# Kernel tuning notes

Measured on AMD Instinct MI355X. Metric: run time of the kernel, lower is better.

Reference implementation:

```python
import jax, jax.numpy as jnp
import numpy as np

N, NC, G, C = 80000, 8000, 16, 5
E, ES = 160000, 80000
NUM_OPS, OP_E, OP_F, CFG_F, H = 120, 32, 140, 18, 32
ALPHA = 0.2  # tf.nn.leaky_relu default slope

seg = jax.ops.segment_sum

def lrelu(x):
    return jnp.where(x >= 0, x, ALPHA * x)

def l2norm(x):
    s = jnp.sum(x * x, axis=-1, keepdims=True)
    return x * jax.lax.rsqrt(jnp.maximum(s, 1e-12))

def setup_inputs():
    k = jax.random.split(jax.random.key(0), 20)
    p = lambda i, shp, s=0.1: jax.random.normal(k[i], shp, jnp.float32) * s
    d_in = CFG_F + OP_F + OP_E  # 190: concat(config, op feats, op embed)
    d_gc = CFG_F + H            # 50: concat(config, hidden)
    return {
        'op_feats': jax.random.normal(k[0], (N, OP_F), jnp.float32),
        'config_feats': jax.random.normal(k[1], (NC, C, CFG_F), jnp.float32),
        'op_ids': jax.random.randint(k[2], (N,), 0, NUM_OPS),
        'selected': jax.random.randint(k[3], (N,), 0, 2) == 1,
        'feed_src': jax.random.randint(k[4], (E,), 0, N),
        'feed_dst': jax.random.randint(k[5], (E,), 0, N),
        'sfeed_src': jax.random.randint(k[6], (ES,), 0, N),
        'sfeed_dst': jax.random.randint(k[7], (ES,), 0, N),
        'config_src': jnp.arange(NC),
        'config_dst': jax.random.randint(k[8], (NC,), 0, N),
        'sconfig_src': jnp.arange(NC),
        'sconfig_dst': jax.random.randint(k[9], (NC,), 0, N),
        'op_gid': (jnp.arange(N) * G) // N,
        'cfg_gid': (jnp.arange(NC) * G) // NC,
        'emb': p(10, (NUM_OPS, OP_E), 1.0),
        'pre_w1': p(11, (d_in, H)), 'pre_b1': jnp.zeros((H,), jnp.float32),
        'pre_w2': p(12, (H, H)), 'pre_b2': jnp.zeros((H,), jnp.float32),
        'gc1_w1': p(13, (d_gc, H)), 'gc1_b1': jnp.zeros((H,), jnp.float32),
        'gc1_w2': p(14, (H, H)), 'gc1_b2': jnp.zeros((H,), jnp.float32),
        'gc2_w1': p(15, (d_gc, H)), 'gc2_b1': jnp.zeros((H,), jnp.float32),
        'gc2_w2': p(16, (H, H)), 'gc2_b2': jnp.zeros((H,), jnp.float32),
        'post_w1': p(17, (3 * H, H)),
        'post_w2': p(18, (H, 1)),
    }

def _mlp(x, w1, b1, w2, b2):
    return lrelu(x @ w1 + b1) @ w2 + b2

def _node_forward(nf, cf, src, dst, csrc, cdst, pre, gcs):
    # AdjacencyMultiplier('config') @ config_feats : scatter nconfig feats to ops
    cfg = 100.0 * seg(cf[csrc], cdst, num_segments=N)            # [N, C, 18]
    x = jnp.broadcast_to(nf[:, None, :], (N, C, nf.shape[-1]))   # stack over configs
    x = lrelu(_mlp(jnp.concatenate([cfg, x], -1), *pre))         # prenet + leaky_relu
    # A_hat = A + A^T + I with symmetric normalization D^-1/2 A_hat D^-1/2
    loop = jnp.arange(N)
    src_all = jnp.concatenate([src, dst, loop])
    dst_all = jnp.concatenate([dst, src, loop])
    inv = jax.lax.rsqrt(seg(jnp.ones(src_all.shape, nf.dtype), dst_all, num_segments=N))
    inv = inv[:, None, None]
    for gp in gcs:
        y = jnp.concatenate([cfg, x], -1) * inv
        y = seg(y[src_all], dst_all, num_segments=N) * inv       # A_hat_norm @ y
        x = x + lrelu(_mlp(y, *gp))                              # residual
    return x

def _forward(op_feats, config_feats, emb, pre, gc1, gc2, post_w1, post_w2,
             op_ids, selected, feed, sfeed, cfg_e, scfg_e, op_gid, cfg_gid):
    nf = jnp.concatenate([op_feats, emb[op_ids]], -1)            # [N, 172]
    x_full = _node_forward(jax.lax.stop_gradient(nf), jax.lax.stop_gradient(config_feats),
                           feed[0], feed[1], cfg_e[0], cfg_e[1], pre, (gc1, gc2))
    x_bp = _node_forward(nf, config_feats, sfeed[0], sfeed[1],
                         scfg_e[0], scfg_e[1], pre, (gc1, gc2))
    x = jnp.where(selected[:, None, None], x_bp, x_full)         # [N, C, H]
    cfg_nodes = seg(x[cfg_e[1]], cfg_e[0], num_segments=NC)      # adj_config^T @ x
    op_sum = seg(x, op_gid, num_segments=G)                      # [G, C, H]
    cnt = seg(jnp.ones((N,), x.dtype), op_gid, num_segments=G)
    op_mean = op_sum / cnt[:, None, None]
    cfg_sum = seg(cfg_nodes, cfg_gid, num_segments=G)
    feats = jnp.concatenate([op_mean, l2norm(op_sum), l2norm(cfg_sum)], -1)  # [G, C, 3H]
    return (lrelu(feats @ post_w1) @ post_w2)[..., 0]            # [G, C]

def reference(op_feats, config_feats, op_ids, selected, feed_src, feed_dst,
              sfeed_src, sfeed_dst, config_src, config_dst, sconfig_src, sconfig_dst,
              op_gid, cfg_gid, emb, pre_w1, pre_b1, pre_w2, pre_b2,
              gc1_w1, gc1_b1, gc1_w2, gc1_b2, gc2_w1, gc2_b1, gc2_w2, gc2_b2,
              post_w1, post_w2):
    return _forward(op_feats, config_feats, emb,
                    (pre_w1, pre_b1, pre_w2, pre_b2),
                    (gc1_w1, gc1_b1, gc1_w2, gc1_b2),
                    (gc2_w1, gc2_b1, gc2_w2, gc2_b2),
                    post_w1, post_w2,
                    op_ids, selected, (feed_src, feed_dst), (sfeed_src, sfeed_dst),
                    (config_src, config_dst), (sconfig_src, sconfig_dst), op_gid, cfg_gid)
```

## Files before the change

### kernel.cpp

```cpp
#include <hip/hip_runtime.h>
#include <hip/hip_bf16.h>
#include <math.h>

#define CDIV(a,b) (((a)+(b)-1)/(b))

constexpr int N_   = 80000;
constexpr int NC_  = 8000;
constexpr int G_   = 16;
constexpr int C_   = 5;
constexpr int CFGF = 18;
constexpr int OPF  = 140;
constexpr int OPE  = 32;
constexpr int H_   = 32;
constexpr int NUMOPS = 120;
constexpr int CROW = C_ * CFGF;
constexpr int XROW = C_ * H_;
constexpr float ALPHA_ = 0.2f;

__device__ __forceinline__ float lrelu(float v) { return v >= 0.0f ? v : ALPHA_ * v; }

__global__ void k_nfwop(const float* __restrict__ emb, const float* __restrict__ w1,
                        const float* __restrict__ b1, float* __restrict__ nfwop) {
    int t = blockIdx.x * blockDim.x + threadIdx.x;
    if (t >= NUMOPS * H_) return;
    int op = t >> 5, h = t & 31;
    float a = b1[h];
    for (int e = 0; e < OPE; ++e)
        a = fmaf(emb[op * OPE + e], w1[(CFGF + OPF + e) * H_ + h], a);
    nfwop[t] = a;
}

__global__ void k_nfw(const float* __restrict__ opf, const int* __restrict__ op_ids,
                      const float* __restrict__ nfwop, const float* __restrict__ w1,
                      float* __restrict__ nfw) {
    int n = blockIdx.x * blockDim.x + threadIdx.x;
    if (n >= N_) return;
    float acc[H_];
    const float4* it = (const float4*)(nfwop + (size_t)op_ids[n] * H_);
    #pragma unroll
    for (int q = 0; q < 8; ++q) {
        float4 v = it[q];
        acc[4 * q + 0] = v.x; acc[4 * q + 1] = v.y; acc[4 * q + 2] = v.z; acc[4 * q + 3] = v.w;
    }
    const float4* f4 = (const float4*)(opf + (size_t)n * OPF);
    const float* wf = w1 + CFGF * H_;
    for (int kc = 0; kc < OPF / 4; ++kc) {
        float4 rv = f4[kc];
        float rs[4] = {rv.x, rv.y, rv.z, rv.w};
        #pragma unroll
        for (int j = 0; j < 4; ++j) {
            int k = kc * 4 + j;
            #pragma unroll
            for (int h = 0; h < H_; ++h) acc[h] = fmaf(rs[j], wf[k * H_ + h], acc[h]);
        }
    }
    float4* o = (float4*)(nfw + (size_t)n * H_);
    #pragma unroll
    for (int q = 0; q < 8; ++q)
        o[q] = make_float4(acc[4 * q], acc[4 * q + 1], acc[4 * q + 2], acc[4 * q + 3]);
}

__global__ void k_cfg_scatter(const float* __restrict__ cf, const int* __restrict__ csrc,
                              const int* __restrict__ cdst, float* __restrict__ cfg) {
    int t = blockIdx.x * blockDim.x + threadIdx.x;
    if (t >= NC_ * CROW) return;
    int i = t / CROW, j = t - i * CROW;
    int s = csrc[i], d = cdst[i];
    atomicAdd(&cfg[(size_t)d * CROW + j], 100.0f * cf[(size_t)s * CROW + j]);
}

__global__ void k_deg(const int* __restrict__ src, const int* __restrict__ dst,
                      int E, int* __restrict__ deg) {
    int e = blockIdx.x * blockDim.x + threadIdx.x;
    if (e >= E) return;
    atomicAdd(&deg[src[e]], 1);
    atomicAdd(&deg[dst[e]], 1);
}

__global__ void k_inv(const int* __restrict__ deg, float* __restrict__ inv) {
    int n = blockIdx.x * blockDim.x + threadIdx.x;
    if (n >= N_) return;
    inv[n] = 1.0f / sqrtf((float)(deg[n] + 1));
}

__global__ void k_scan1(const int* __restrict__ deg, int* __restrict__ roff, int* __restrict__ aux) {
    __shared__ int s[256];
    int t = threadIdx.x, n = blockIdx.x * 256 + t;
    int v = (n < N_) ? deg[n] : 0;
    s[t] = v; __syncthreads();
    for (int off = 1; off < 256; off <<= 1) {
        int x = (t >= off) ? s[t - off] : 0;
        __syncthreads();
        s[t] += x;
        __syncthreads();
    }
    if (n < N_) roff[n] = s[t] - v;
    if (t == 255) aux[blockIdx.x] = s[255];
}

__global__ void k_scan2(int* __restrict__ aux, int nb) {
    __shared__ int s[512];
    int t = threadIdx.x;
    int v = (t < nb) ? aux[t] : 0;
    s[t] = v; __syncthreads();
    for (int off = 1; off < 512; off <<= 1) {
        int x = (t >= off) ? s[t - off] : 0;
        __syncthreads();
        s[t] += x;
        __syncthreads();
    }
    if (t < nb) aux[t] = s[t] - v;
}

__global__ void k_scan3(int* __restrict__ roff, const int* __restrict__ aux,
                        int* __restrict__ cur, int total) {
    int n = blockIdx.x * blockDim.x + threadIdx.x;
    if (n < N_) {
        int r = roff[n] + aux[n >> 8];
        roff[n] = r;
        cur[n] = r;
    }
    if (n == 0) roff[N_] = total;
}

__global__ void k_fill(const int* __restrict__ src, const int* __restrict__ dst, int E,
                       int* __restrict__ cur, int* __restrict__ col) {
    int e = blockIdx.x * blockDim.x + threadIdx.x;
    if (e >= E) return;
    int s = src[e], d = dst[e];
    col[atomicAdd(&cur[d], 1)] = s;
    col[atomicAdd(&cur[s], 1)] = d;
}

__global__ void k_csum_gather(const float2* __restrict__ cfg2, const float* __restrict__ inv,
                              const int* __restrict__ roff, const int* __restrict__ col,
                              float2* __restrict__ csum2) {
    int t = blockIdx.x * blockDim.x + threadIdx.x;
    if (t >= N_ * 45) return;
    int n = t / 45, j2 = t - n * 45;
    float iv = inv[n];
    float2 a = cfg2[t];
    a.x *= iv; a.y *= iv;
    int p1 = roff[n + 1];
    for (int p = roff[n]; p < p1; ++p) {
        int s = col[p];
        float ivs = inv[s];
        float2 v = cfg2[(size_t)s * 45 + j2];
        a.x = fmaf(v.x, ivs, a.x);
        a.y = fmaf(v.y, ivs, a.y);
    }
    csum2[t] = a;
}

__global__ void k_pre(const float* __restrict__ cfg, const float* __restrict__ nfw,
                      const float* __restrict__ w1, const float* __restrict__ w2,
                      const float* __restrict__ b2, float* __restrict__ x) {
    int r = blockIdx.x * blockDim.x + threadIdx.x;
    if (r >= N_ * C_) return;
    int n = r / C_;
    float h1[H_];
    const float4* nf4 = (const float4*)(nfw + (size_t)n * H_);
    #pragma unroll
    for (int q = 0; q < 8; ++q) {
        float4 v = nf4[q];
        h1[4 * q + 0] = v.x; h1[4 * q + 1] = v.y; h1[4 * q + 2] = v.z; h1[4 * q + 3] = v.w;
    }
    const float2* c2 = (const float2*)(cfg + (size_t)r * CFGF);
    for (int kc = 0; kc < CFGF / 2; ++kc) {
        float2 cv = c2[kc];
        float cs[2] = {cv.x, cv.y};
        #pragma unroll
        for (int j = 0; j < 2; ++j) {
            int k = kc * 2 + j;
            #pragma unroll
            for (int h = 0; h < H_; ++h) h1[h] = fmaf(cs[j], w1[k * H_ + h], h1[h]);
        }
    }
    #pragma unroll
    for (int h = 0; h < H_; ++h) h1[h] = lrelu(h1[h]);
    float acc[H_];
    #pragma unroll
    for (int h = 0; h < H_; ++h) acc[h] = b2[h];
    #pragma unroll
    for (int k = 0; k < H_; ++k) {
        float v = h1[k];
        #pragma unroll
        for (int h = 0; h < H_; ++h) acc[h] = fmaf(v, w2[k * H_ + h], acc[h]);
    }
    float4* o = (float4*)(x + (size_t)r * H_);
    #pragma unroll
    for (int q = 0; q < 8; ++q)
        o[q] = make_float4(lrelu(acc[4 * q]), lrelu(acc[4 * q + 1]),
                           lrelu(acc[4 * q + 2]), lrelu(acc[4 * q + 3]));
}

__global__ void k_gcfused(const float4* __restrict__ xin4, const float* __restrict__ csum,
                          const float* __restrict__ inv, const int* __restrict__ roff,
                          const int* __restrict__ col,
                          const float* __restrict__ w1, const float* __restrict__ b1,
                          const float* __restrict__ w2, const float* __restrict__ b2,
                          float4* __restrict__ xout4) {
    int r = blockIdx.x * blockDim.x + threadIdx.x;
    if (r >= N_ * C_) return;
    int n = r / C_, c = r - n * C_;
    float iv = inv[n];
    float xs[H_];
    const float4* sp = xin4 + (size_t)r * 8;
    #pragma unroll
    for (int q = 0; q < 8; ++q) {
        float4 v = sp[q];
        xs[4 * q + 0] = v.x * iv; xs[4 * q + 1] = v.y * iv;
        xs[4 * q + 2] = v.z * iv; xs[4 * q + 3] = v.w * iv;
    }
    int p1 = roff[n + 1];
    for (int p = roff[n]; p < p1; ++p) {
        int s = col[p];
        float ivs = inv[s];
        const float4* np = xin4 + ((size_t)s * C_ + c) * 8;
        #pragma unroll
        for (int q = 0; q < 8; ++q) {
            float4 v = np[q];
            xs[4 * q + 0] = fmaf(v.x, ivs, xs[4 * q + 0]);
            xs[4 * q + 1] = fmaf(v.y, ivs, xs[4 * q + 1]);
            xs[4 * q + 2] = fmaf(v.z, ivs, xs[4 * q + 2]);
            xs[4 * q + 3] = fmaf(v.w, ivs, xs[4 * q + 3]);
        }
    }
    float t1[H_];
    #pragma unroll
    for (int h = 0; h < H_; ++h) t1[h] = 0.0f;
    const float2* c2 = (const float2*)(csum + (size_t)r * CFGF);
    for (int kc = 0; kc < CFGF / 2; ++kc) {
        float2 cv = c2[kc];
        float cs[2] = {cv.x, cv.y};
        #pragma unroll
        for (int j = 0; j < 2; ++j) {
            int k = kc * 2 + j;
            #pragma unroll
            for (int h = 0; h < H_; ++h) t1[h] = fmaf(cs[j], w1[k * H_ + h], t1[h]);
        }
    }
    #pragma unroll
    for (int k = 0; k < H_; ++k) {
        float v = xs[k];
        #pragma unroll
        for (int h = 0; h < H_; ++h) t1[h] = fmaf(v, w1[(CFGF + k) * H_ + h], t1[h]);
    }
    float h1[H_];
    #pragma unroll
    for (int h = 0; h < H_; ++h) h1[h] = lrelu(fmaf(iv, t1[h], b1[h]));
    float acc[H_];
    #pragma unroll
    for (int h = 0; h < H_; ++h) acc[h] = b2[h];
    #pragma unroll
    for (int k = 0; k < H_; ++k) {
        float v = h1[k];
        #pragma unroll
        for (int h = 0; h < H_; ++h) acc[h] = fmaf(v, w2[k * H_ + h], acc[h]);
    }
    float4* o = xout4 + (size_t)r * 8;
    #pragma unroll
    for (int q = 0; q < 8; ++q) {
        float4 v = sp[q];
        v.x += lrelu(acc[4 * q + 0]); v.y += lrelu(acc[4 * q + 1]);
        v.z += lrelu(acc[4 * q + 2]); v.w += lrelu(acc[4 * q + 3]);
        o[q] = v;
    }
}

__global__ void k_opsum(const float4* __restrict__ xf4, const float4* __restrict__ xb4,
                        const int* __restrict__ sel, const int* __restrict__ gid,
                        float* __restrict__ osum, float* __restrict__ cnt) {
    __shared__ float4 ls[6 * G_ * 40];
    __shared__ float lc[6 * G_];
    for (int i = threadIdx.x; i < 6 * G_ * 40; i += blockDim.x) ls[i] = make_float4(0.f, 0.f, 0.f, 0.f);
    if (threadIdx.x < 6 * G_) lc[threadIdx.x] = 0.0f;
    __syncthreads();
    int j4 = threadIdx.x % 40, i = threadIdx.x / 40;
    const int NPB = CDIV(N_, 512);
    int start = blockIdx.x * NPB;
    int end = min(start + NPB, N_);
    if (i < 6) {
        for (int n = start + i; n < end; n += 6) {
            int g = gid[n];
            const float4* xr = sel[n] ? xb4 : xf4;
            float4 v = xr[(size_t)n * 40 + j4];
            int o = (i * G_ + g) * 40 + j4;
            float4 c = ls[o];
            c.x += v.x; c.y += v.y; c.z += v.z; c.w += v.w;
            ls[o] = c;
            if (j4 == 0) lc[i * G_ + g] += 1.0f;
        }
    }
    __syncthreads();
    for (int idx = threadIdx.x; idx < G_ * 40; idx += blockDim.x) {
        float4 s = ls[idx];
        #pragma unroll
        for (int q = 1; q < 6; ++q) {
            float4 v = ls[q * G_ * 40 + idx];
            s.x += v.x; s.y += v.y; s.z += v.z; s.w += v.w;
        }
        int g = idx / 40, j = idx - g * 40;
        float* o = osum + (size_t)g * XROW + j * 4;
        atomicAdd(o + 0, s.x); atomicAdd(o + 1, s.y);
        atomicAdd(o + 2, s.z); atomicAdd(o + 3, s.w);
    }
    if (threadIdx.x < G_) {
        float c = 0.0f;
        #pragma unroll
        for (int q = 0; q < 6; ++q) c += lc[q * G_ + threadIdx.x];
        atomicAdd(&cnt[threadIdx.x], c);
    }
}

__global__ void k_cfgsum(const float4* __restrict__ xf4, const float4* __restrict__ xb4,
                         const int* __restrict__ sel, const int* __restrict__ csrc,
                         const int* __restrict__ cdst, const int* __restrict__ cfg_gid,
                         float* __restrict__ gsum) {
    __shared__ float4 ls[6 * G_ * 40];
    for (int i = threadIdx.x; i < 6 * G_ * 40; i += blockDim.x) ls[i] = make_float4(0.f, 0.f, 0.f, 0.f);
    __syncthreads();
    int j4 = threadIdx.x % 40, i = threadIdx.x / 40;
    const int EPB = CDIV(NC_, 64);
    int start = blockIdx.x * EPB;
    int end = min(start + EPB, NC_);
    if (i < 6) {
        for (int e = start + i; e < end; e += 6) {
            int g = cfg_gid[csrc[e]];
            int n = cdst[e];
            const float4* xr = sel[n] ? xb4 : xf4;
            float4 v = xr[(size_t)n * 40 + j4];
            int o = (i * G_ + g) * 40 + j4;
            float4 c = ls[o];
            c.x += v.x; c.y += v.y; c.z += v.z; c.w += v.w;
            ls[o] = c;
        }
    }
    __syncthreads();
    for (int idx = threadIdx.x; idx < G_ * 40; idx += blockDim.x) {
        float4 s = ls[idx];
        #pragma unroll
        for (int q = 1; q < 6; ++q) {
            float4 v = ls[q * G_ * 40 + idx];
            s.x += v.x; s.y += v.y; s.z += v.z; s.w += v.w;
        }
        int g = idx / 40, j = idx - g * 40;
        float* o = gsum + (size_t)g * XROW + j * 4;
        atomicAdd(o + 0, s.x); atomicAdd(o + 1, s.y);
        atomicAdd(o + 2, s.z); atomicAdd(o + 3, s.w);
    }
}

__global__ void k_final(const float* __restrict__ osum, const float* __restrict__ gsum,
                        const float* __restrict__ cnt, const float* __restrict__ pw1,
                        const float* __restrict__ pw2, float* __restrict__ out) {
    __shared__ float sw1[3 * H_ * H_];
    __shared__ float sw2[H_];
    for (int i = threadIdx.x; i < 3 * H_ * H_; i += blockDim.x) sw1[i] = pw1[i];
    if (threadIdx.x < H_) sw2[threadIdx.x] = pw2[threadIdx.x];
    __syncthreads();
    int t = threadIdx.x;
    if (t >= G_ * C_) return;
    int g = t / C_;
    const float* os = osum + (size_t)t * H_;
    const float* cs = gsum + (size_t)t * H_;
    float icnt = 1.0f / cnt[g];
    float a0[H_], a1[H_], a2[H_];
    float s1 = 0.0f, s2 = 0.0f;
    #pragma unroll
    for (int h = 0; h < H_; ++h) {
        float v1 = os[h], v2 = cs[h];
        a0[h] = v1 * icnt;
        a1[h] = v1; s1 = fmaf(v1, v1, s1);
        a2[h] = v2; s2 = fmaf(v2, v2, s2);
    }
    float r1 = 1.0f / sqrtf(fmaxf(s1, 1e-12f));
    float r2 = 1.0f / sqrtf(fmaxf(s2, 1e-12f));
    #pragma unroll
    for (int h = 0; h < H_; ++h) { a1[h] *= r1; a2[h] *= r2; }
    float o = 0.0f;
    #pragma unroll
    for (int h = 0; h < H_; ++h) {
        float a = 0.0f;
        #pragma unroll
        for (int k = 0; k < H_; ++k) a = fmaf(a0[k], sw1[k * H_ + h], a);
        #pragma unroll
        for (int k = 0; k < H_; ++k) a = fmaf(a1[k], sw1[(H_ + k) * H_ + h], a);
        #pragma unroll
        for (int k = 0; k < H_; ++k) a = fmaf(a2[k], sw1[(2 * H_ + k) * H_ + h], a);
        o = fmaf(lrelu(a), sw2[h], o);
    }
    out[t] = o;
}

extern "C" void kernel_launch(void* const* d_in, const int* in_sizes, int n_in,
                              void* d_out, int out_size, void* d_ws, size_t ws_size,
                              hipStream_t stream) {
    const float* op_feats     = (const float*)d_in[0];
    const float* config_feats = (const float*)d_in[1];
    const int*   op_ids       = (const int*)d_in[2];
    const int*   selected     = (const int*)d_in[3];
    const int*   feed_src     = (const int*)d_in[4];
    const int*   feed_dst     = (const int*)d_in[5];
    const int*   sfeed_src    = (const int*)d_in[6];
    const int*   sfeed_dst    = (const int*)d_in[7];
    const int*   config_src   = (const int*)d_in[8];
    const int*   config_dst   = (const int*)d_in[9];
    const int*   sconfig_src  = (const int*)d_in[10];
    const int*   sconfig_dst  = (const int*)d_in[11];
    const int*   op_gid       = (const int*)d_in[12];
    const int*   cfg_gid      = (const int*)d_in[13];
    const float* emb          = (const float*)d_in[14];
    const float* pre_w1       = (const float*)d_in[15];
    const float* pre_b1       = (const float*)d_in[16];
    const float* pre_w2       = (const float*)d_in[17];
    const float* pre_b2       = (const float*)d_in[18];
    const float* gc_w1[2]     = {(const float*)d_in[19], (const float*)d_in[23]};
    const float* gc_b1[2]     = {(const float*)d_in[20], (const float*)d_in[24]};
    const float* gc_w2[2]     = {(const float*)d_in[21], (const float*)d_in[25]};
    const float* gc_b2[2]     = {(const float*)d_in[22], (const float*)d_in[26]};
    const float* post_w1      = (const float*)d_in[27];
    const float* post_w2      = (const float*)d_in[28];

    char* ws = (char*)d_ws;
    size_t off = 0;
    auto alloc = [&](size_t bytes) { void* p = ws + off; off += (bytes + 255) & ~(size_t)255; return p; };
    float* nfw  = (float*)alloc((size_t)N_ * H_ * 4);
    float* nfwop= (float*)alloc((size_t)NUMOPS * H_ * 4);
    float* cfg  = (float*)alloc((size_t)N_ * CROW * 4);
    float* inv  = (float*)alloc((size_t)N_ * 4);
    int*   deg  = (int*)alloc((size_t)N_ * 4);
    float* xf   = (float*)alloc((size_t)N_ * XROW * 4);
    float* xb   = (float*)alloc((size_t)N_ * XROW * 4);
    float* csum = (float*)alloc((size_t)N_ * CROW * 4);
    float* xscr = (float*)alloc((size_t)N_ * XROW * 4);
    int*   roff = (int*)alloc((size_t)(N_ + 1) * 4);
    int*   cur  = (int*)alloc((size_t)N_ * 4);
    int*   aux  = (int*)alloc((size_t)512 * 4);
    int*   col  = (int*)alloc((size_t)2 * 160000 * 4);
    float* osum = (float*)alloc((size_t)G_ * XROW * 4);
    float* gsum = (float*)alloc((size_t)G_ * XROW * 4);
    float* cntb = (float*)alloc((size_t)G_ * 4);

    const int NB1 = CDIV(N_, 256);

    k_nfwop<<<CDIV(NUMOPS * H_, 256), 256, 0, stream>>>(emb, pre_w1, pre_b1, nfwop);
    k_nfw<<<CDIV(N_, 256), 256, 0, stream>>>(op_feats, op_ids, nfwop, pre_w1, nfw);

    for (int fwd = 0; fwd < 2; ++fwd) {
        const int* esrc = fwd ? sfeed_src : feed_src;
        const int* edst = fwd ? sfeed_dst : feed_dst;
        int Ecur = fwd ? in_sizes[6] : in_sizes[4];
        const int* csrc = fwd ? sconfig_src : config_src;
        const int* cdst = fwd ? sconfig_dst : config_dst;
        float* x0 = fwd ? xb : xf;

        hipMemsetAsync(cfg, 0, (size_t)N_ * CROW * 4, stream);
        hipMemsetAsync(deg, 0, (size_t)N_ * 4, stream);
        k_cfg_scatter<<<CDIV(NC_ * CROW, 256), 256, 0, stream>>>(config_feats, csrc, cdst, cfg);
        k_deg<<<CDIV(Ecur, 256), 256, 0, stream>>>(esrc, edst, Ecur, deg);
        k_inv<<<CDIV(N_, 256), 256, 0, stream>>>(deg, inv);
        k_scan1<<<NB1, 256, 0, stream>>>(deg, roff, aux);
        k_scan2<<<1, 512, 0, stream>>>(aux, NB1);
        k_scan3<<<CDIV(N_, 256), 256, 0, stream>>>(roff, aux, cur, 2 * Ecur);
        k_fill<<<CDIV(Ecur, 256), 256, 0, stream>>>(esrc, edst, Ecur, cur, col);

        k_csum_gather<<<CDIV(N_ * 45, 256), 256, 0, stream>>>((const float2*)cfg, inv, roff, col,
                                                              (float2*)csum);
        k_pre<<<CDIV(N_ * C_, 256), 256, 0, stream>>>(cfg, nfw, pre_w1, pre_w2, pre_b2, x0);

        k_gcfused<<<CDIV(N_ * C_, 256), 256, 0, stream>>>((const float4*)x0, csum, inv, roff, col,
                                                          gc_w1[0], gc_b1[0], gc_w2[0], gc_b2[0],
                                                          (float4*)xscr);
        k_gcfused<<<CDIV(N_ * C_, 256), 256, 0, stream>>>((const float4*)xscr, csum, inv, roff, col,
                                                          gc_w1[1], gc_b1[1], gc_w2[1], gc_b2[1],
                                                          (float4*)x0);
    }

    hipMemsetAsync(osum, 0, (size_t)G_ * XROW * 4, stream);
    hipMemsetAsync(gsum, 0, (size_t)G_ * XROW * 4, stream);
    hipMemsetAsync(cntb, 0, (size_t)G_ * 4, stream);
    k_opsum<<<512, 256, 0, stream>>>((const float4*)xf, (const float4*)xb, selected, op_gid, osum, cntb);
    k_cfgsum<<<64, 256, 0, stream>>>((const float4*)xf, (const float4*)xb, selected,
                                     config_src, config_dst, cfg_gid, gsum);
    k_final<<<1, 128, 0, stream>>>(osum, gsum, cntb, post_w1, post_w2, (float*)d_out);
}
```

Before: 751.6 us.

## Map one thread per hidden unit with shared-memory weights for pre and GC MLPs

Replaces the thread-per-row pre-MLP and graph-conv kernels with versions where each warp-sized group of 32 threads handles one row, one thread per hidden channel. Weights and per-row config features are staged in shared memory, and intermediate activations go through shared memory between layers. Neighbor gathers become coalesced 128-byte reads instead of per-thread strided float4 loads, and the large per-thread register arrays are gone. In exchange every block reloads the weights into shared memory for only 8 rows, and the kernels add block-wide barriers.

```diff
diff --git a/kernel.cpp b/kernel.cpp
--- a/kernel.cpp
+++ b/kernel.cpp
@@ -15,6 +15,7 @@
 constexpr int NUMOPS = 120;
 constexpr int CROW = C_ * CFGF;
 constexpr int XROW = C_ * H_;
+constexpr int DGC  = CFGF + H_;
 constexpr float ALPHA_ = 0.2f;
 
 __device__ __forceinline__ float lrelu(float v) { return v >= 0.0f ? v : ALPHA_ * v; }
@@ -152,120 +153,74 @@
     csum2[t] = a;
 }
 
-__global__ void k_pre(const float* __restrict__ cfg, const float* __restrict__ nfw,
-                      const float* __restrict__ w1, const float* __restrict__ w2,
-                      const float* __restrict__ b2, float* __restrict__ x) {
-    int r = blockIdx.x * blockDim.x + threadIdx.x;
-    if (r >= N_ * C_) return;
+__global__ void k_pre32(const float* __restrict__ cfg, const float* __restrict__ nfw,
+                        const float* __restrict__ w1, const float* __restrict__ w2,
+                        const float* __restrict__ b2, float* __restrict__ x) {
+    __shared__ float sw1[CFGF * H_];
+    __shared__ float sw2[H_ * H_];
+    __shared__ float scfg[8][CFGF];
+    __shared__ float sh1[8][H_];
+    int tid = threadIdx.x;
+    int base = blockIdx.x * 8;
+    for (int i = tid; i < CFGF * H_; i += 256) sw1[i] = w1[i];
+    for (int i = tid; i < H_ * H_; i += 256) sw2[i] = w2[i];
+    if (tid < 8 * CFGF) scfg[tid / CFGF][tid % CFGF] = cfg[(size_t)base * CFGF + tid];
+    __syncthreads();
+    int rl = tid >> 5, h = tid & 31;
+    int r = base + rl;
     int n = r / C_;
-    float h1[H_];
-    const float4* nf4 = (const float4*)(nfw + (size_t)n * H_);
-    #pragma unroll
-    for (int q = 0; q < 8; ++q) {
-        float4 v = nf4[q];
-        h1[4 * q + 0] = v.x; h1[4 * q + 1] = v.y; h1[4 * q + 2] = v.z; h1[4 * q + 3] = v.w;
-    }
-    const float2* c2 = (const float2*)(cfg + (size_t)r * CFGF);
-    for (int kc = 0; kc < CFGF / 2; ++kc) {
-        float2 cv = c2[kc];
-        float cs[2] = {cv.x, cv.y};
-        #pragma unroll
-        for (int j = 0; j < 2; ++j) {
-            int k = kc * 2 + j;
-            #pragma unroll
-            for (int h = 0; h < H_; ++h) h1[h] = fmaf(cs[j], w1[k * H_ + h], h1[h]);
-        }
-    }
-    #pragma unroll
-    for (int h = 0; h < H_; ++h) h1[h] = lrelu(h1[h]);
-    float acc[H_];
-    #pragma unroll
-    for (int h = 0; h < H_; ++h) acc[h] = b2[h];
-    #pragma unroll
-    for (int k = 0; k < H_; ++k) {
-        float v = h1[k];
-        #pragma unroll
-        for (int h = 0; h < H_; ++h) acc[h] = fmaf(v, w2[k * H_ + h], acc[h]);
-    }
-    float4* o = (float4*)(x + (size_t)r * H_);
-    #pragma unroll
-    for (int q = 0; q < 8; ++q)
-        o[q] = make_float4(lrelu(acc[4 * q]), lrelu(acc[4 * q + 1]),
-                           lrelu(acc[4 * q + 2]), lrelu(acc[4 * q + 3]));
-}
-
-__global__ void k_gcfused(const float4* __restrict__ xin4, const float* __restrict__ csum,
-                          const float* __restrict__ inv, const int* __restrict__ roff,
-                          const int* __restrict__ col,
-                          const float* __restrict__ w1, const float* __restrict__ b1,
-                          const float* __restrict__ w2, const float* __restrict__ b2,
-                          float4* __restrict__ xout4) {
-    int r = blockIdx.x * blockDim.x + threadIdx.x;
-    if (r >= N_ * C_) return;
+    float a = nfw[(size_t)n * H_ + h];
+    #pragma unroll
+    for (int k = 0; k < CFGF; ++k) a = fmaf(scfg[rl][k], sw1[k * H_ + h], a);
+    sh1[rl][h] = lrelu(a);
+    __syncthreads();
+    float acc = b2[h];
+    #pragma unroll
+    for (int k = 0; k < H_; ++k) acc = fmaf(sh1[rl][k], sw2[k * H_ + h], acc);
+    x[(size_t)r * H_ + h] = lrelu(acc);
+}
+
+__global__ void k_gc32(const float* __restrict__ xin, const float* __restrict__ csum,
+                       const float* __restrict__ inv, const int* __restrict__ roff,
+                       const int* __restrict__ col,
+                       const float* __restrict__ w1, const float* __restrict__ b1,
+                       const float* __restrict__ w2, const float* __restrict__ b2,
+                       float* __restrict__ xout) {
+    __shared__ float sw1[DGC * H_];
+    __shared__ float sw2[H_ * H_];
+    __shared__ float scs[8][CFGF];
+    __shared__ float sxs[8][H_];
+    __shared__ float sh1[8][H_];
+    int tid = threadIdx.x;
+    int base = blockIdx.x * 8;
+    for (int i = tid; i < DGC * H_; i += 256) sw1[i] = w1[i];
+    for (int i = tid; i < H_ * H_; i += 256) sw2[i] = w2[i];
+    if (tid < 8 * CFGF) scs[tid / CFGF][tid % CFGF] = csum[(size_t)base * CFGF + tid];
+    __syncthreads();
+    int rl = tid >> 5, h = tid & 31;
+    int r = base + rl;
     int n = r / C_, c = r - n * C_;
     float iv = inv[n];
-    float xs[H_];
-    const float4* sp = xin4 + (size_t)r * 8;
-    #pragma unroll
-    for (int q = 0; q < 8; ++q) {
-        float4 v = sp[q];
-        xs[4 * q + 0] = v.x * iv; xs[4 * q + 1] = v.y * iv;
-        xs[4 * q + 2] = v.z * iv; xs[4 * q + 3] = v.w * iv;
-    }
+    float xself = xin[(size_t)r * H_ + h];
+    float xs = iv * xself;
     int p1 = roff[n + 1];
     for (int p = roff[n]; p < p1; ++p) {
         int s = col[p];
-        float ivs = inv[s];
-        const float4* np = xin4 + ((size_t)s * C_ + c) * 8;
-        #pragma unroll
-        for (int q = 0; q < 8; ++q) {
-            float4 v = np[q];
-            xs[4 * q + 0] = fmaf(v.x, ivs, xs[4 * q + 0]);
-            xs[4 * q + 1] = fmaf(v.y, ivs, xs[4 * q + 1]);
-            xs[4 * q + 2] = fmaf(v.z, ivs, xs[4 * q + 2]);
-            xs[4 * q + 3] = fmaf(v.w, ivs, xs[4 * q + 3]);
-        }
-    }
-    float t1[H_];
-    #pragma unroll
-    for (int h = 0; h < H_; ++h) t1[h] = 0.0f;
-    const float2* c2 = (const float2*)(csum + (size_t)r * CFGF);
-    for (int kc = 0; kc < CFGF / 2; ++kc) {
-        float2 cv = c2[kc];
-        float cs[2] = {cv.x, cv.y};
-        #pragma unroll
-        for (int j = 0; j < 2; ++j) {
-            int k = kc * 2 + j;
-            #pragma unroll
-            for (int h = 0; h < H_; ++h) t1[h] = fmaf(cs[j], w1[k * H_ + h], t1[h]);
-        }
-    }
-    #pragma unroll
-    for (int k = 0; k < H_; ++k) {
-        float v = xs[k];
-        #pragma unroll
-        for (int h = 0; h < H_; ++h) t1[h] = fmaf(v, w1[(CFGF + k) * H_ + h], t1[h]);
-    }
-    float h1[H_];
-    #pragma unroll
-    for (int h = 0; h < H_; ++h) h1[h] = lrelu(fmaf(iv, t1[h], b1[h]));
-    float acc[H_];
-    #pragma unroll
-    for (int h = 0; h < H_; ++h) acc[h] = b2[h];
-    #pragma unroll
-    for (int k = 0; k < H_; ++k) {
-        float v = h1[k];
-        #pragma unroll
-        for (int h = 0; h < H_; ++h) acc[h] = fmaf(v, w2[k * H_ + h], acc[h]);
-    }
-    float4* o = xout4 + (size_t)r * 8;
-    #pragma unroll
-    for (int q = 0; q < 8; ++q) {
-        float4 v = sp[q];
-        v.x += lrelu(acc[4 * q + 0]); v.y += lrelu(acc[4 * q + 1]);
-        v.z += lrelu(acc[4 * q + 2]); v.w += lrelu(acc[4 * q + 3]);
-        o[q] = v;
-    }
+        xs = fmaf(inv[s], xin[((size_t)s * C_ + c) * H_ + h], xs);
+    }
+    sxs[rl][h] = xs;
+    float t1 = 0.0f;
+    #pragma unroll
+    for (int k = 0; k < CFGF; ++k) t1 = fmaf(scs[rl][k], sw1[k * H_ + h], t1);
+    __syncthreads();
+    #pragma unroll
+    for (int k = 0; k < H_; ++k) t1 = fmaf(sxs[rl][k], sw1[(CFGF + k) * H_ + h], t1);
+    sh1[rl][h] = lrelu(fmaf(iv, t1, b1[h]));
+    __syncthreads();
+    float acc = b2[h];
+    #pragma unroll
+    for (int k = 0; k < H_; ++k) acc = fmaf(sh1[rl][k], sw2[k * H_ + h], acc);
+    xout[(size_t)r * H_ + h] = xself + lrelu(acc);
 }
 
 __global__ void k_opsum(const float4* __restrict__ xf4, const float4* __restrict__ xb4,
@@ -443,6 +398,7 @@
     float* cntb = (float*)alloc((size_t)G_ * 4);
 
     const int NB1 = CDIV(N_, 256);
+    const int NROWB = CDIV(N_ * C_, 8);
 
     k_nfwop<<<CDIV(NUMOPS * H_, 256), 256, 0, stream>>>(emb, pre_w1, pre_b1, nfwop);
     k_nfw<<<CDIV(N_, 256), 256, 0, stream>>>(op_feats, op_ids, nfwop, pre_w1, nfw);
@@ -467,14 +423,12 @@
 
         k_csum_gather<<<CDIV(N_ * 45, 256), 256, 0, stream>>>((const float2*)cfg, inv, roff, col,
                                                               (float2*)csum);
-        k_pre<<<CDIV(N_ * C_, 256), 256, 0, stream>>>(cfg, nfw, pre_w1, pre_w2, pre_b2, x0);
-
-        k_gcfused<<<CDIV(N_ * C_, 256), 256, 0, stream>>>((const float4*)x0, csum, inv, roff, col,
-                                                          gc_w1[0], gc_b1[0], gc_w2[0], gc_b2[0],
-                                                          (float4*)xscr);
-        k_gcfused<<<CDIV(N_ * C_, 256), 256, 0, stream>>>((const float4*)xscr, csum, inv, roff, col,
-                                                          gc_w1[1], gc_b1[1], gc_w2[1], gc_b2[1],
-                                                          (float4*)x0);
+        k_pre32<<<NROWB, 256, 0, stream>>>(cfg, nfw, pre_w1, pre_w2, pre_b2, x0);
+
+        k_gc32<<<NROWB, 256, 0, stream>>>(x0, csum, inv, roff, col,
+                                          gc_w1[0], gc_b1[0], gc_w2[0], gc_b2[0], xscr);
+        k_gc32<<<NROWB, 256, 0, stream>>>(xscr, csum, inv, roff, col,
+                                          gc_w1[1], gc_b1[1], gc_w2[1], gc_b2[1], x0);
     }
 
     hipMemsetAsync(osum, 0, (size_t)G_ * XROW * 4, stream);
```

New measurement: 1.225 ms. +62.9%, slower.

## Remap graph-conv and config gather kernels to one wavefront per node

Applied to the files above, without the earlier changes.

The graph-conv kernel changes from one thread per (node, config) row, which held 32-wide register arrays and gathered float4 rows, to one 64-lane wavefront per node. Each lane owns one hidden unit for up to three configs. Neighbor rows are read coalesced across lanes, weights are staged in shared memory, and the two small matmuls are done per lane from LDS. The config-sum gather is likewise remapped to one wavefront per node with neighbors unrolled by two. The aim is fewer scattered uncoalesced loads and less register pressure, at the cost of idle lanes (45/64 and 5/6 utilization), per-block weight reloads and block-wide syncs.

```diff
diff --git a/kernel.cpp b/kernel.cpp
--- a/kernel.cpp
+++ b/kernel.cpp
@@ -15,6 +15,7 @@
 constexpr int NUMOPS = 120;
 constexpr int CROW = C_ * CFGF;
 constexpr int XROW = C_ * H_;
+constexpr int DGC  = CFGF + H_;
 constexpr float ALPHA_ = 0.2f;
 
 __device__ __forceinline__ float lrelu(float v) { return v >= 0.0f ? v : ALPHA_ * v; }
@@ -132,24 +133,37 @@
     col[atomicAdd(&cur[s], 1)] = d;
 }
 
-__global__ void k_csum_gather(const float2* __restrict__ cfg2, const float* __restrict__ inv,
-                              const int* __restrict__ roff, const int* __restrict__ col,
-                              float2* __restrict__ csum2) {
-    int t = blockIdx.x * blockDim.x + threadIdx.x;
-    if (t >= N_ * 45) return;
-    int n = t / 45, j2 = t - n * 45;
+__global__ void k_csum_w(const float2* __restrict__ cfg2, const float* __restrict__ inv,
+                         const int* __restrict__ roff, const int* __restrict__ col,
+                         float2* __restrict__ csum2) {
+    int tid = threadIdx.x;
+    int w = tid >> 6, lane = tid & 63;
+    int n = blockIdx.x * 4 + w;
     float iv = inv[n];
-    float2 a = cfg2[t];
-    a.x *= iv; a.y *= iv;
-    int p1 = roff[n + 1];
-    for (int p = roff[n]; p < p1; ++p) {
-        int s = col[p];
-        float ivs = inv[s];
-        float2 v = cfg2[(size_t)s * 45 + j2];
-        a.x = fmaf(v.x, ivs, a.x);
-        a.y = fmaf(v.y, ivs, a.y);
-    }
-    csum2[t] = a;
+    bool act = lane < 45;
+    size_t self = (size_t)n * 45 + lane;
+    float2 a = make_float2(0.f, 0.f);
+    if (act) { a = cfg2[self]; a.x *= iv; a.y *= iv; }
+    int e = roff[n], p1 = roff[n + 1];
+    for (; e + 1 < p1; e += 2) {
+        int s0 = col[e], s1 = col[e + 1];
+        float i0 = inv[s0], i1 = inv[s1];
+        if (act) {
+            float2 v0 = cfg2[(size_t)s0 * 45 + lane];
+            float2 v1 = cfg2[(size_t)s1 * 45 + lane];
+            a.x = fmaf(v0.x, i0, a.x); a.y = fmaf(v0.y, i0, a.y);
+            a.x = fmaf(v1.x, i1, a.x); a.y = fmaf(v1.y, i1, a.y);
+        }
+    }
+    if (e < p1) {
+        int s0 = col[e];
+        float i0 = inv[s0];
+        if (act) {
+            float2 v0 = cfg2[(size_t)s0 * 45 + lane];
+            a.x = fmaf(v0.x, i0, a.x); a.y = fmaf(v0.y, i0, a.y);
+        }
+    }
+    if (act) csum2[self] = a;
 }
 
 __global__ void k_pre(const float* __restrict__ cfg, const float* __restrict__ nfw,
@@ -194,77 +208,89 @@
                            lrelu(acc[4 * q + 2]), lrelu(acc[4 * q + 3]));
 }
 
-__global__ void k_gcfused(const float4* __restrict__ xin4, const float* __restrict__ csum,
-                          const float* __restrict__ inv, const int* __restrict__ roff,
-                          const int* __restrict__ col,
-                          const float* __restrict__ w1, const float* __restrict__ b1,
-                          const float* __restrict__ w2, const float* __restrict__ b2,
-                          float4* __restrict__ xout4) {
-    int r = blockIdx.x * blockDim.x + threadIdx.x;
-    if (r >= N_ * C_) return;
-    int n = r / C_, c = r - n * C_;
+__global__ void k_gcnode(const float* __restrict__ xin, const float* __restrict__ csum,
+                         const float* __restrict__ inv, const int* __restrict__ roff,
+                         const int* __restrict__ col,
+                         const float* __restrict__ w1, const float* __restrict__ b1,
+                         const float* __restrict__ w2, const float* __restrict__ b2,
+                         float* __restrict__ xout) {
+    __shared__ float sw1[DGC * H_];
+    __shared__ float sw2[H_ * H_];
+    __shared__ float scs[4][CROW];
+    __shared__ float sxs[4][C_][H_];
+    __shared__ float sh1[4][C_][H_];
+    int tid = threadIdx.x;
+    for (int i = tid; i < DGC * H_; i += 256) sw1[i] = w1[i];
+    for (int i = tid; i < H_ * H_; i += 256) sw2[i] = w2[i];
+    int w = tid >> 6, lane = tid & 63;
+    int c0 = lane >> 5, h = lane & 31;
+    int n = blockIdx.x * 4 + w;
+    for (int i = lane; i < CROW; i += 64) scs[w][i] = csum[(size_t)n * CROW + i];
     float iv = inv[n];
-    float xs[H_];
-    const float4* sp = xin4 + (size_t)r * 8;
-    #pragma unroll
-    for (int q = 0; q < 8; ++q) {
-        float4 v = sp[q];
-        xs[4 * q + 0] = v.x * iv; xs[4 * q + 1] = v.y * iv;
-        xs[4 * q + 2] = v.z * iv; xs[4 * q + 3] = v.w * iv;
-    }
-    int p1 = roff[n + 1];
-    for (int p = roff[n]; p < p1; ++p) {
-        int s = col[p];
-        float ivs = inv[s];
-        const float4* np = xin4 + ((size_t)s * C_ + c) * 8;
-        #pragma unroll
-        for (int q = 0; q < 8; ++q) {
-            float4 v = np[q];
-            xs[4 * q + 0] = fmaf(v.x, ivs, xs[4 * q + 0]);
-            xs[4 * q + 1] = fmaf(v.y, ivs, xs[4 * q + 1]);
-            xs[4 * q + 2] = fmaf(v.z, ivs, xs[4 * q + 2]);
-            xs[4 * q + 3] = fmaf(v.w, ivs, xs[4 * q + 3]);
-        }
-    }
-    float t1[H_];
-    #pragma unroll
-    for (int h = 0; h < H_; ++h) t1[h] = 0.0f;
-    const float2* c2 = (const float2*)(csum + (size_t)r * CFGF);
-    for (int kc = 0; kc < CFGF / 2; ++kc) {
-        float2 cv = c2[kc];
-        float cs[2] = {cv.x, cv.y};
-        #pragma unroll
-        for (int j = 0; j < 2; ++j) {
-            int k = kc * 2 + j;
+    const float* xrow = xin + (size_t)n * XROW;
+    float xself[3], xs[3];
+    #pragma unroll
+    for (int p = 0; p < 3; ++p) {
+        int c = 2 * p + c0;
+        xself[p] = (c < C_) ? xrow[c * H_ + h] : 0.0f;
+        xs[p] = iv * xself[p];
+    }
+    int e = roff[n], p1 = roff[n + 1];
+    for (; e + 1 < p1; e += 2) {
+        int s0 = col[e], s1 = col[e + 1];
+        float i0 = inv[s0], i1 = inv[s1];
+        const float* r0 = xin + (size_t)s0 * XROW;
+        const float* r1 = xin + (size_t)s1 * XROW;
+        #pragma unroll
+        for (int p = 0; p < 3; ++p) {
+            int c = 2 * p + c0;
+            float v0 = (c < C_) ? r0[c * H_ + h] : 0.0f;
+            float v1 = (c < C_) ? r1[c * H_ + h] : 0.0f;
+            xs[p] = fmaf(i0, v0, xs[p]);
+            xs[p] = fmaf(i1, v1, xs[p]);
+        }
+    }
+    if (e < p1) {
+        int s0 = col[e];
+        float i0 = inv[s0];
+        const float* r0 = xin + (size_t)s0 * XROW;
+        #pragma unroll
+        for (int p = 0; p < 3; ++p) {
+            int c = 2 * p + c0;
+            float v0 = (c < C_) ? r0[c * H_ + h] : 0.0f;
+            xs[p] = fmaf(i0, v0, xs[p]);
+        }
+    }
+    #pragma unroll
+    for (int p = 0; p < 3; ++p) {
+        int c = 2 * p + c0;
+        if (c < C_) sxs[w][c][h] = xs[p];
+    }
+    __syncthreads();
+    float h1v[3];
+    #pragma unroll
+    for (int p = 0; p < 3; ++p) {
+        int c = 2 * p + c0;
+        if (c < C_) {
+            float t1 = 0.0f;
             #pragma unroll
-            for (int h = 0; h < H_; ++h) t1[h] = fmaf(cs[j], w1[k * H_ + h], t1[h]);
-        }
-    }
-    #pragma unroll
-    for (int k = 0; k < H_; ++k) {
-        float v = xs[k];
-        #pragma unroll
-        for (int h = 0; h < H_; ++h) t1[h] = fmaf(v, w1[(CFGF + k) * H_ + h], t1[h]);
-    }
-    float h1[H_];
-    #pragma unroll
-    for (int h = 0; h < H_; ++h) h1[h] = lrelu(fmaf(iv, t1[h], b1[h]));
-    float acc[H_];
-    #pragma unroll
-    for (int h = 0; h < H_; ++h) acc[h] = b2[h];
-    #pragma unroll
-    for (int k = 0; k < H_; ++k) {
-        float v = h1[k];
-        #pragma unroll
-        for (int h = 0; h < H_; ++h) acc[h] = fmaf(v, w2[k * H_ + h], acc[h]);
-    }
-    float4* o = xout4 + (size_t)r * 8;
-    #pragma unroll
-    for (int q = 0; q < 8; ++q) {
-        float4 v = sp[q];
-        v.x += lrelu(acc[4 * q + 0]); v.y += lrelu(acc[4 * q + 1]);
-        v.z += lrelu(acc[4 * q + 2]); v.w += lrelu(acc[4 * q + 3]);
-        o[q] = v;
+            for (int f = 0; f < CFGF; ++f) t1 = fmaf(scs[w][c * CFGF + f], sw1[f * H_ + h], t1);
+            #pragma unroll
+            for (int k = 0; k < H_; ++k) t1 = fmaf(sxs[w][c][k], sw1[(CFGF + k) * H_ + h], t1);
+            h1v[p] = lrelu(fmaf(iv, t1, b1[h]));
+            sh1[w][c][h] = h1v[p];
+        }
+    }
+    __syncthreads();
+    #pragma unroll
+    for (int p = 0; p < 3; ++p) {
+        int c = 2 * p + c0;
+        if (c < C_) {
+            float acc = b2[h];
+            #pragma unroll
+            for (int k = 0; k < H_; ++k) acc = fmaf(sh1[w][c][k], sw2[k * H_ + h], acc);
+            xout[((size_t)n * C_ + c) * H_ + h] = xself[p] + lrelu(acc);
+        }
     }
 }
 
@@ -443,6 +469,7 @@
     float* cntb = (float*)alloc((size_t)G_ * 4);
 
     const int NB1 = CDIV(N_, 256);
+    const int NODEB = N_ / 4;
 
     k_nfwop<<<CDIV(NUMOPS * H_, 256), 256, 0, stream>>>(emb, pre_w1, pre_b1, nfwop);
     k_nfw<<<CDIV(N_, 256), 256, 0, stream>>>(op_feats, op_ids, nfwop, pre_w1, nfw);
@@ -465,16 +492,13 @@
         k_scan3<<<CDIV(N_, 256), 256, 0, stream>>>(roff, aux, cur, 2 * Ecur);
         k_fill<<<CDIV(Ecur, 256), 256, 0, stream>>>(esrc, edst, Ecur, cur, col);
 
-        k_csum_gather<<<CDIV(N_ * 45, 256), 256, 0, stream>>>((const float2*)cfg, inv, roff, col,
-                                                              (float2*)csum);
+        k_csum_w<<<NODEB, 256, 0, stream>>>((const float2*)cfg, inv, roff, col, (float2*)csum);
         k_pre<<<CDIV(N_ * C_, 256), 256, 0, stream>>>(cfg, nfw, pre_w1, pre_w2, pre_b2, x0);
 
-        k_gcfused<<<CDIV(N_ * C_, 256), 256, 0, stream>>>((const float4*)x0, csum, inv, roff, col,
-                                                          gc_w1[0], gc_b1[0], gc_w2[0], gc_b2[0],
-                                                          (float4*)xscr);
-        k_gcfused<<<CDIV(N_ * C_, 256), 256, 0, stream>>>((const float4*)xscr, csum, inv, roff, col,
-                                                          gc_w1[1], gc_b1[1], gc_w2[1], gc_b2[1],
-                                                          (float4*)x0);
+        k_gcnode<<<NODEB, 256, 0, stream>>>(x0, csum, inv, roff, col,
+                                            gc_w1[0], gc_b1[0], gc_w2[0], gc_b2[0], xscr);
+        k_gcnode<<<NODEB, 256, 0, stream>>>(xscr, csum, inv, roff, col,
+                                            gc_w1[1], gc_b1[1], gc_w2[1], gc_b2[1], x0);
     }
 
     hipMemsetAsync(osum, 0, (size_t)G_ * XROW * 4, stream);
```

After: 902.5 us. +20.1%, slower.
